# Optimization experiments

Measured on AMD Instinct MI355X. Metric: run time of the kernel, lower is better.

The kernel has to match this reference:

```python
import jax, jax.numpy as jnp
import numpy as np

N_NODES = 370
N_EEG = 64
HID = 64
L = 8
KS = 2
EMB = 16
KTOP = N_NODES // 10  # 37, as in the torch code


def _gcn_norm_dense(A):
    # A[dst, src] dense adjacency. torch_geometric GCNConv gcn_norm:
    # add self-loop weight 1.0 only for nodes lacking one, then D^-1/2 A D^-1/2.
    d0 = jnp.diagonal(A)
    A = A + jnp.diag(jnp.where(d0 > 0, 0.0, 1.0))
    deg = A.sum(axis=1)  # weighted in-degree at dst (incl. self loops)
    dinv = jnp.where(deg > 0, jax.lax.rsqrt(deg), 0.0)
    return dinv[:, None] * A * dinv[None, :]


def _adaptive_adj(emb_src, emb_tgt):
    # softmax(relu(S T^T)) row-wise, keep top-k per row (softmax vals are all >0)
    adj = jax.nn.softmax(jax.nn.relu(emb_src @ emb_tgt.T), axis=-1)
    vals, idx = jax.lax.top_k(adj, KTOP)
    sp = jnp.zeros_like(adj).at[jnp.arange(adj.shape[0])[:, None], idx].set(vals)
    return _gcn_norm_dense(sp)


def _causal_conv(h, w, b, dilation):
    # h: (BN, H, T), w: (H_out, H_in, K); left-pad by (K-1)*dilation => causal
    pad = (w.shape[-1] - 1) * dilation
    out = jax.lax.conv_general_dilated(
        h, w, window_strides=(1,), padding=[(pad, 0)],
        rhs_dilation=(dilation,), dimension_numbers=("NCH", "OIH", "NCH"))
    return out + b[None, :, None]


def _layernorm(x, g, b, eps=1e-5):
    m = x.mean(-1, keepdims=True)
    v = ((x - m) ** 2).mean(-1, keepdims=True)
    return (x - m) * jax.lax.rsqrt(v + eps) * g + b


def _gelu(x):
    return jax.nn.gelu(x, approximate=False)


def setup_inputs() -> dict:
    key = jax.random.key(0)
    ks = iter(jax.random.split(key, 64))
    B, T, E = 8, 64, 7400

    x = jax.random.normal(next(ks), (B, T, N_NODES, HID), jnp.float32)
    src = jax.random.randint(next(ks), (E,), 0, N_NODES, jnp.int32)
    off = jax.random.randint(next(ks), (E,), 1, N_NODES, jnp.int32)
    edge_index = jnp.stack([src, (src + off) % N_NODES])  # self-loop free
    edge_weight = jax.random.uniform(next(ks), (E,), jnp.float32)

    def rn(shape, scale):
        return jax.random.normal(next(ks), shape, jnp.float32) * scale

    s = 1.0 / np.sqrt(HID)
    inp = {
        "x": x, "edge_index": edge_index, "edge_weight": edge_weight,
        "in_W": rn((HID, HID), s), "in_b": rn((HID,), 0.01),
        "gcnf_W": rn((L, HID, HID), s), "gcnf_b": rn((L, HID), 0.01),
        "emb_src": rn((L, N_NODES, EMB), 1.0),  # torch.randn init
        "emb_tgt": rn((L, N_NODES, EMB), 1.0),
        "gcna_W": rn((L, HID, HID), s), "gcna_b": rn((L, HID), 0.01),
        "filt_W": rn((L, HID, HID, KS), s), "filt_b": rn((L, HID), 0.01),
        "gate_W": rn((L, HID, HID, KS), s), "gate_b": rn((L, HID), 0.01),
        "res_W": rn((L, HID, HID), s), "res_b": rn((L, HID), 0.01),
        "skip_W": rn((L, HID, HID), s), "skip_b": rn((L, HID), 0.01),
        "ln_g": jnp.ones((L, HID), jnp.float32), "ln_b": jnp.zeros((L, HID), jnp.float32),
        "end1_W": rn((HID, HID), s), "end1_b": rn((HID,), 0.01),
        "end2_W": rn((HID, HID), s), "end2_b": rn((HID,), 0.01),
        "eeg1_W": rn((N_NODES * HID, 256), 1.0 / np.sqrt(N_NODES * HID)), "eeg1_b": rn((256,), 0.01),
        "eeg2_W": rn((256, N_EEG), 1.0 / 16.0), "eeg2_b": rn((N_EEG,), 0.01),
    }
    return inp


def reference(x, edge_index, edge_weight, in_W, in_b, gcnf_W, gcnf_b,
              emb_src, emb_tgt, gcna_W, gcna_b, filt_W, filt_b, gate_W, gate_b,
              res_W, res_b, skip_W, skip_b, ln_g, ln_b,
              end1_W, end1_b, end2_W, end2_b, eeg1_W, eeg1_b, eeg2_W, eeg2_b):
    B, T, N, H = x.shape
    x = x @ in_W + in_b  # input_proj

    # Fixed (DTI prior) adjacency: same for every layer, build & normalize once.
    A = jnp.zeros((N, N), x.dtype).at[edge_index[1], edge_index[0]].add(edge_weight)
    A = _gcn_norm_dense(A)

    skip_sum = jnp.zeros_like(x)
    for i in range(L):  # fixed small layer count
        dil = 2 ** (i % 4)
        xf = x.reshape(B * T, N, H)
        h_fixed = jnp.einsum("mn,bnh->bmh", A, xf @ gcnf_W[i]) + gcnf_b[i]
        Aa = _adaptive_adj(emb_src[i], emb_tgt[i])
        h_adapt = jnp.einsum("mn,bnh->bmh", Aa, xf @ gcna_W[i]) + gcna_b[i]
        h = (h_fixed + h_adapt).reshape(B, T, N, H)
        h = h.transpose(0, 2, 3, 1).reshape(B * N, H, T)
        h = jnp.tanh(_causal_conv(h, filt_W[i], filt_b[i], dil)) * \
            jax.nn.sigmoid(_causal_conv(h, gate_W[i], gate_b[i], dil))
        # 1x1 convs over channel dim (dropout is identity in eval)
        skip = (jnp.einsum("oi,nit->not", skip_W[i], h) + skip_b[i][None, :, None])
        res = (jnp.einsum("oi,nit->not", res_W[i], h) + res_b[i][None, :, None])
        skip = skip.reshape(B, N, H, T).transpose(0, 3, 1, 2)
        res = res.reshape(B, N, H, T).transpose(0, 3, 1, 2)
        x = _layernorm(res + x, ln_g[i], ln_b[i])
        skip_sum = skip_sum + skip

    h = _gelu(skip_sum) @ end1_W + end1_b
    h = _gelu(h) @ end2_W + end2_b
    h = h.reshape(B, T, N * H)  # GraphToEEG
    h = _gelu(h @ eeg1_W + eeg1_b) @ eeg2_W + eeg2_b
    return h
```

## Files before the change

kernel.cpp:

```cpp
#include <hip/hip_runtime.h>
#include <hip/hip_bf16.h>
#include <math.h>

typedef __attribute__((ext_vector_type(8))) short bf16x8;
typedef __attribute__((ext_vector_type(4))) float f32x4;
typedef unsigned short u16;
typedef unsigned int u32;
typedef unsigned long long u64;

#define NN 370
#define HH 64
#define LL 8
#define TT 64
#define BTOT 512
#define RR (BTOT*NN)
#define KTOPK 37
#define SPLITK 37

__device__ inline u16 f2bf(float f){
  __hip_bfloat16 h = __float2bfloat16(f);
  return __builtin_bit_cast(u16, h);
}
__device__ inline float bf2f(short s){
  u32 v = ((u32)(u16)s) << 16;
  return __builtin_bit_cast(float, v);
}
__device__ inline float gelu_f(float x){ return 0.5f * x * (1.0f + erff(x * 0.70710678118654752440f)); }

__device__ inline void sts16(char* lds, int row, int kb, int stride, bf16x8 v){
  *reinterpret_cast<bf16x8*>(lds + row*stride + (kb ^ ((row&7)<<4))) = v;
}
__device__ inline bf16x8 lds16(const char* lds, int row, int kb, int stride){
  return *reinterpret_cast<const bf16x8*>(lds + row*stride + (kb ^ ((row&7)<<4)));
}
__device__ inline bf16x8 gldB(const char* Bt, int c, int kb, int stride){
  return *reinterpret_cast<const bf16x8*>(Bt + c*stride + (kb ^ ((c&7)<<4)));
}

__global__ void kzero(float* __restrict__ p, size_t n){
  for(size_t i = (size_t)blockIdx.x*256 + threadIdx.x; i < n; i += (size_t)gridDim.x*256) p[i] = 0.f;
}

__global__ void kbuildA(const int* __restrict__ ei, const float* __restrict__ ew, float* __restrict__ Araw, int E){
  int e = blockIdx.x*256 + threadIdx.x;
  if(e < E){
    int src = ei[e], dst = ei[E + e];
    atomicAdd(&Araw[dst*NN + src], ew[e]);
  }
}

__global__ __launch_bounds__(64) void knormF(float* __restrict__ Araw, float* __restrict__ dinvF){
  int i = blockIdx.x, ln = threadIdx.x;
  float d0 = Araw[i*NN + i];
  float s = 0.f;
  for(int j = ln; j < NN; j += 64) s += Araw[i*NN + j];
#pragma unroll
  for(int o=1;o<64;o<<=1) s += __shfl_xor(s, o, 64);
  if(ln == 0){
    if(d0 == 0.f){ Araw[i*NN+i] = 1.f; s += 1.f; }
    dinvF[i] = rsqrtf(s);
  }
}

__global__ __launch_bounds__(512) void kadapt(const float* __restrict__ esrc, const float* __restrict__ etgt,
                                              float* __restrict__ ArawA, float* __restrict__ dinvA){
  __shared__ float tgT[16][372];
  __shared__ float red[8];
  __shared__ u64 keys[512];
  __shared__ int diagflag;
  int i = blockIdx.x, l = blockIdx.y, tid = threadIdx.x;
  const float* Et = etgt + (size_t)l*NN*16;
  for(int idx = tid; idx < NN*16; idx += 512)
    tgT[idx & 15][idx >> 4] = Et[idx];
  float sr[16];
  const float* Es = esrc + ((size_t)l*NN + i)*16;
#pragma unroll
  for(int k=0;k<16;k++) sr[k] = Es[k];
  if(tid == 0) diagflag = 0;
  __syncthreads();
  bool act = tid < NN;
  float s = 0.f;
  if(act){
    float d = 0.f;
#pragma unroll
    for(int k=0;k<16;k++) d += sr[k]*tgT[k][tid];
    s = fmaxf(d, 0.f);
  }
  float v = act ? s : -1.f;
#pragma unroll
  for(int o=1;o<64;o<<=1) v = fmaxf(v, __shfl_xor(v,o,64));
  if((tid&63)==0) red[tid>>6] = v;
  __syncthreads();
  float mx = red[0];
#pragma unroll
  for(int q=1;q<8;q++) mx = fmaxf(mx, red[q]);
  __syncthreads();
  float e = act ? expf(s - mx) : 0.f;
  float t = e;
#pragma unroll
  for(int o=1;o<64;o<<=1) t += __shfl_xor(t,o,64);
  if((tid&63)==0) red[tid>>6] = t;
  __syncthreads();
  float sum = 0.f;
#pragma unroll
  for(int q=0;q<8;q++) sum += red[q];
  float p = e / sum;
  u32 fb = __builtin_bit_cast(u32, p);
  keys[tid] = act ? ((((u64)fb)<<32) | (u64)(0xFFFFFFFFu - (u32)tid)) : 0ULL;
  __syncthreads();
  for(int k2=2; k2<=512; k2<<=1){
    for(int j=k2>>1; j>0; j>>=1){
      int ixj = tid ^ j;
      if(ixj > tid){
        u64 a = keys[tid], b = keys[ixj];
        bool dirUp = ((tid & k2) == 0);
        if(dirUp ? (a < b) : (a > b)){ keys[tid] = b; keys[ixj] = a; }
      }
      __syncthreads();
    }
  }
  float myval = 0.f; int myidx = -1;
  if(tid < KTOPK){
    u64 kk = keys[tid];
    myidx = (int)(0xFFFFFFFFu - (u32)kk);
    myval = __builtin_bit_cast(float, (u32)(kk>>32));
    if(myidx == i) diagflag = 1;
  }
  __syncthreads();
  float dsum = (tid < KTOPK) ? myval : 0.f;
  if(tid < 64){
#pragma unroll
    for(int o=1;o<64;o<<=1) dsum += __shfl_xor(dsum,o,64);
    if(tid == 0) dinvA[l*NN + i] = rsqrtf(dsum + (diagflag ? 0.f : 1.f));
  }
  if(tid < KTOPK) ArawA[((size_t)l*NN + i)*NN + myidx] = myval;
  if(tid == 0 && !diagflag) ArawA[((size_t)l*NN + i)*NN + i] = 1.f;
}

__global__ void kacat(const float* __restrict__ Araw, const float* __restrict__ ArawA,
                      const float* __restrict__ dinvF, const float* __restrict__ dinvA,
                      u16* __restrict__ Acat){
  int idx = blockIdx.x*256 + threadIdx.x;
  if(idx >= LL*384*768) return;
  int k = idx % 768; int m = (idx / 768) % 384; int l = idx / (768*384);
  float v = 0.f;
  if(m < NN){
    if(k < 384){
      if(k < NN) v = dinvF[m]*Araw[m*NN+k]*dinvF[k];
    } else {
      int n = k - 384;
      if(n < NN) v = dinvA[l*NN+m]*ArawA[((size_t)l*NN+m)*NN+n]*dinvA[l*NN+n];
    }
  }
  Acat[idx] = f2bf(v);
}

__global__ void kbt_small(const float* __restrict__ inW, const float* __restrict__ e1W, const float* __restrict__ e2W,
                          u16* __restrict__ BtIN, u16* __restrict__ BtE1, u16* __restrict__ BtE2){
  const float* W = blockIdx.x==0 ? inW : (blockIdx.x==1 ? e1W : e2W);
  u16* Bt = blockIdx.x==0 ? BtIN : (blockIdx.x==1 ? BtE1 : BtE2);
  for(int idx = threadIdx.x; idx < 4096; idx += 256){
    int c = idx >> 6, k = idx & 63;
    *(u16*)((char*)Bt + c*128 + ((k*2) ^ ((c&7)<<4))) = f2bf(W[k*64 + c]);
  }
}

__global__ void kbt_layer(const float* __restrict__ gcnfW, const float* __restrict__ gcnaW,
                          const float* __restrict__ filtW, const float* __restrict__ gateW,
                          const float* __restrict__ skipW, const float* __restrict__ resW,
                          u16* __restrict__ BtUV, u16* __restrict__ BtCV, u16* __restrict__ BtSR){
  int l = blockIdx.x, which = blockIdx.y;
  if(which == 0){
    u16* Bt = BtUV + (size_t)l*128*64;
    for(int idx=threadIdx.x; idx<8192; idx+=256){
      int c = idx>>6, k = idx&63;
      float v = (c<64) ? gcnfW[(size_t)l*4096 + k*64 + c] : gcnaW[(size_t)l*4096 + k*64 + (c-64)];
      *(u16*)((char*)Bt + c*128 + ((k*2) ^ ((c&7)<<4))) = f2bf(v);
    }
  } else if(which == 1){
    u16* Bt = BtCV + (size_t)l*128*128;
    for(int idx=threadIdx.x; idx<16384; idx+=256){
      int c = idx>>7, k = idx&127;
      const float* W = (c<64) ? filtW : gateW;
      int o = c & 63, ii = k & 63, tap = (k<64) ? 1 : 0;
      float v = W[(size_t)l*8192 + o*128 + ii*2 + tap];
      *(u16*)((char*)Bt + c*256 + ((k*2) ^ ((c&7)<<4))) = f2bf(v);
    }
  } else {
    u16* Bt = BtSR + (size_t)l*128*64;
    for(int idx=threadIdx.x; idx<8192; idx+=256){
      int c = idx>>6, k = idx&63;
      float v = (c<64) ? skipW[(size_t)l*4096 + c*64 + k] : resW[(size_t)l*4096 + (c-64)*64 + k];
      *(u16*)((char*)Bt + c*128 + ((k*2) ^ ((c&7)<<4))) = f2bf(v);
    }
  }
}

__global__ void ktrans(const float* __restrict__ W, u16* __restrict__ Wt){
  __shared__ float tile[64][65];
  int kb = blockIdx.x*64, cb = blockIdx.y*64;
  for(int idx = threadIdx.x; idx < 4096; idx += 256){
    int kk = idx>>6, cc = idx&63;
    tile[kk][cc] = W[(size_t)(kb+kk)*256 + cb+cc];
  }
  __syncthreads();
  for(int idx = threadIdx.x; idx < 4096; idx += 256){
    int cc = idx>>6, kk = idx&63;
    Wt[(size_t)(cb+cc)*23680 + kb+kk] = f2bf(tile[kk][cc]);
  }
}

__global__ __launch_bounds__(256) void krowmm_in(const float* __restrict__ X, const u16* __restrict__ Bt,
                                                 const float* __restrict__ bias,
                                                 u16* __restrict__ xbf){
  int tid = threadIdx.x;
  int w = tid>>6, ln = tid&63, lr = ln&15, hi = ln>>4;
  int kboff = hi<<4;
  size_t r = (size_t)blockIdx.x*64 + w*16 + lr;
  f32x4 acc[4];
#pragma unroll
  for(int i=0;i<4;i++) acc[i] = f32x4{0.f,0.f,0.f,0.f};
  const char* BI = (const char*)Bt;
#pragma unroll
  for(int kt=0; kt<2; ++kt){
    const float* xr = X + r*64 + kt*32 + hi*8;
    float4 pa = ((const float4*)xr)[0], pb = ((const float4*)xr)[1];
    bf16x8 a;
    a[0]=(short)f2bf(pa.x); a[1]=(short)f2bf(pa.y); a[2]=(short)f2bf(pa.z); a[3]=(short)f2bf(pa.w);
    a[4]=(short)f2bf(pb.x); a[5]=(short)f2bf(pb.y); a[6]=(short)f2bf(pb.z); a[7]=(short)f2bf(pb.w);
#pragma unroll
    for(int nt=0; nt<4; ++nt){
      bf16x8 b = gldB(BI, nt*16 + lr, kt*64 + kboff, 128);
      acc[nt] = __builtin_amdgcn_mfma_f32_16x16x32_bf16(a, b, acc[nt], 0, 0, 0);
    }
  }
  size_t r0 = (size_t)blockIdx.x*64;
#pragma unroll
  for(int nt=0; nt<4; ++nt){
    int c = nt*16 + lr;
    float bv = bias[c];
#pragma unroll
    for(int rr=0;rr<4;++rr){
      int row = w*16 + hi*4 + rr;
      xbf[(r0+row)*64 + c] = f2bf(acc[nt][rr] + bv);
    }
  }
}

__global__ __launch_bounds__(512) void kgcn(const u16* __restrict__ xbf, const u16* __restrict__ BtUV,
                                            const u16* __restrict__ Acat,
                                            const float* __restrict__ bfb, const float* __restrict__ bab,
                                            u16* __restrict__ t2){
  __shared__ char uvt[64*768];
  int bt = blockIdx.x, tid = threadIdx.x;
  int w = tid>>6, ln = tid&63, lr = ln&15, hi = ln>>4;
  int kboff = hi<<4;
  f32x4 acc[12];
#pragma unroll
  for(int j=0;j<12;j++) acc[j] = f32x4{0.f,0.f,0.f,0.f};
  const char* xb = (const char*)(xbf + (size_t)bt*NN*64);
  for(int p=0; p<2; ++p){
    bf16x8 bw[2][4];
#pragma unroll
    for(int kt=0;kt<2;++kt)
#pragma unroll
      for(int nt=0;nt<4;++nt){
        int c = p*64 + nt*16 + lr;
        bw[kt][nt] = *reinterpret_cast<const bf16x8*>((const char*)BtUV + c*128 + ((kt*64 + kboff) ^ ((c&7)<<4)));
      }
    f32x4 uvacc[3][4];
#pragma unroll
    for(int mi=0;mi<3;++mi)
#pragma unroll
      for(int nt=0;nt<4;++nt) uvacc[mi][nt] = f32x4{0.f,0.f,0.f,0.f};
#pragma unroll
    for(int mi=0;mi<3;++mi){
      int node = (w*3+mi)*16 + lr;
#pragma unroll
      for(int kt=0;kt<2;++kt){
        bf16x8 a;
        if(node < NN) a = *reinterpret_cast<const bf16x8*>(xb + (size_t)node*128 + kt*64 + kboff);
        else { bf16x8 z = {0,0,0,0,0,0,0,0}; a = z; }
#pragma unroll
        for(int nt=0;nt<4;++nt)
          uvacc[mi][nt] = __builtin_amdgcn_mfma_f32_16x16x32_bf16(a, bw[kt][nt], uvacc[mi][nt], 0,0,0);
      }
    }
    __syncthreads();
#pragma unroll
    for(int mi=0;mi<3;++mi){
      int nd = (w*3+mi)*16 + hi*4;
#pragma unroll
      for(int nt=0;nt<4;++nt){
        int cl = nt*16 + lr;
        u64 pk = (u64)((u32)f2bf(uvacc[mi][nt][0]) | ((u32)f2bf(uvacc[mi][nt][1])<<16))
               | ((u64)((u32)f2bf(uvacc[mi][nt][2]) | ((u32)f2bf(uvacc[mi][nt][3])<<16)) << 32);
        *(u64*)(uvt + cl*768 + ((nd*2) ^ ((cl&7)<<4))) = pk;
      }
    }
    __syncthreads();
    const char* abase = (const char*)Acat + p*768 + kboff;
    __builtin_amdgcn_s_setprio(1);
#pragma unroll
    for(int kt=0; kt<12; ++kt){
      bf16x8 a0 = *reinterpret_cast<const bf16x8*>(abase + (size_t)((w*3+0)*16 + lr)*1536 + kt*64);
      bf16x8 a1 = *reinterpret_cast<const bf16x8*>(abase + (size_t)((w*3+1)*16 + lr)*1536 + kt*64);
      bf16x8 a2 = *reinterpret_cast<const bf16x8*>(abase + (size_t)((w*3+2)*16 + lr)*1536 + kt*64);
      bf16x8 b0 = lds16(uvt, 0*16 + lr, kt*64 + kboff, 768);
      bf16x8 b1 = lds16(uvt, 1*16 + lr, kt*64 + kboff, 768);
      bf16x8 b2 = lds16(uvt, 2*16 + lr, kt*64 + kboff, 768);
      bf16x8 b3 = lds16(uvt, 3*16 + lr, kt*64 + kboff, 768);
      acc[0]  = __builtin_amdgcn_mfma_f32_16x16x32_bf16(a0, b0, acc[0],  0,0,0);
      acc[1]  = __builtin_amdgcn_mfma_f32_16x16x32_bf16(a0, b1, acc[1],  0,0,0);
      acc[2]  = __builtin_amdgcn_mfma_f32_16x16x32_bf16(a0, b2, acc[2],  0,0,0);
      acc[3]  = __builtin_amdgcn_mfma_f32_16x16x32_bf16(a0, b3, acc[3],  0,0,0);
      acc[4]  = __builtin_amdgcn_mfma_f32_16x16x32_bf16(a1, b0, acc[4],  0,0,0);
      acc[5]  = __builtin_amdgcn_mfma_f32_16x16x32_bf16(a1, b1, acc[5],  0,0,0);
      acc[6]  = __builtin_amdgcn_mfma_f32_16x16x32_bf16(a1, b2, acc[6],  0,0,0);
      acc[7]  = __builtin_amdgcn_mfma_f32_16x16x32_bf16(a1, b3, acc[7],  0,0,0);
      acc[8]  = __builtin_amdgcn_mfma_f32_16x16x32_bf16(a2, b0, acc[8],  0,0,0);
      acc[9]  = __builtin_amdgcn_mfma_f32_16x16x32_bf16(a2, b1, acc[9],  0,0,0);
      acc[10] = __builtin_amdgcn_mfma_f32_16x16x32_bf16(a2, b2, acc[10], 0,0,0);
      acc[11] = __builtin_amdgcn_mfma_f32_16x16x32_bf16(a2, b3, acc[11], 0,0,0);
    }
    __builtin_amdgcn_s_setprio(0);
  }
#pragma unroll
  for(int mi=0; mi<3; ++mi){
    int mt = w*3 + mi;
    int mbase = mt*16 + hi*4;
#pragma unroll
    for(int nt=0; nt<4; ++nt){
      int col = nt*16 + lr;
      float bias = bfb[col] + bab[col];
#pragma unroll
      for(int r=0;r<4;++r){
        int m = mbase + r;
        if(m < NN) t2[((size_t)bt*NN + m)*64 + col] = f2bf(acc[mi*4+nt][r] + bias);
      }
    }
  }
}

__global__ __launch_bounds__(256) void kcsr(const u16* __restrict__ t2, const u16* __restrict__ BtC,
                                            const u16* __restrict__ BtS,
                                            const float* __restrict__ fb, const float* __restrict__ gb,
                                            const float* __restrict__ sb, const float* __restrict__ rb,
                                            const float* __restrict__ lng, const float* __restrict__ lnb,
                                            u16* __restrict__ skip,
                                            u16* __restrict__ xbf, int dil, int first, int douv){
  __shared__ char sA[24576];
  char* sact = sA;
  char* ssr  = sA + 8192;
  int blk = blockIdx.x, tid = threadIdx.x;
  int w = tid>>6, ln = tid&63, lr = ln&15, hi = ln>>4;
  int kboff = hi<<4;
  int r0 = blk*64;
  int r = r0 + w*16 + lr;
  int t = (r / NN) & (TT-1);
  const char* cur = (const char*)t2 + (size_t)r*128;
  const char* prv = cur - (size_t)dil*NN*128;
  bf16x8 a0 = *reinterpret_cast<const bf16x8*>(cur + kboff);
  bf16x8 a1 = *reinterpret_cast<const bf16x8*>(cur + 64 + kboff);
  bf16x8 a2, a3;
  if(t >= dil){
    a2 = *reinterpret_cast<const bf16x8*>(prv + kboff);
    a3 = *reinterpret_cast<const bf16x8*>(prv + 64 + kboff);
  } else {
    bf16x8 z = {0,0,0,0,0,0,0,0}; a2 = z; a3 = z;
  }
  const char* BC = (const char*)BtC;
  f32x4 acc[8];
#pragma unroll
  for(int i=0;i<8;i++) acc[i] = f32x4{0.f,0.f,0.f,0.f};
  bf16x8 afr[4] = {a0, a1, a2, a3};
#pragma unroll
  for(int kt=0; kt<4; ++kt){
    bf16x8 bfr[8];
#pragma unroll
    for(int nt=0; nt<8; ++nt)
      bfr[nt] = gldB(BC, nt*16 + lr, kt*64 + kboff, 256);
#pragma unroll
    for(int nt=0; nt<8; ++nt)
      acc[nt] = __builtin_amdgcn_mfma_f32_16x16x32_bf16(afr[kt], bfr[nt], acc[nt], 0, 0, 0);
  }
  u16 qv[4][4];
#pragma unroll
  for(int nt=0; nt<4; ++nt){
    int o = nt*16 + lr;
    float fbv = fb[o], gbv = gb[o];
#pragma unroll
    for(int rr=0;rr<4;++rr){
      float fv = acc[nt][rr] + fbv;
      float gv = acc[nt+4][rr] + gbv;
      float ef = __expf(-2.f*fv);
      float th = (1.f - ef) * __builtin_amdgcn_rcpf(1.f + ef);
      float sg = __builtin_amdgcn_rcpf(1.f + __expf(-gv));
      qv[nt][rr] = f2bf(th * sg);
    }
  }
#pragma unroll
  for(int nt=0; nt<4; ++nt){
    int col = nt*16 + lr;
#pragma unroll
    for(int rr=0;rr<4;++rr){
      int row = w*16 + hi*4 + rr;
      *(u16*)(sact + row*128 + ((col*2) ^ ((row&7)<<4))) = qv[nt][rr];
    }
  }
  __syncthreads();
  const char* BS = (const char*)BtS;
  f32x4 as[8];
#pragma unroll
  for(int i=0;i<8;i++) as[i] = f32x4{0.f,0.f,0.f,0.f};
#pragma unroll
  for(int kt=0; kt<2; ++kt){
    bf16x8 a = lds16(sact, w*16 + lr, kt*64 + kboff, 128);
    bf16x8 bfr[8];
#pragma unroll
    for(int nt=0; nt<8; ++nt)
      bfr[nt] = gldB(BS, nt*16 + lr, kt*64 + kboff, 128);
#pragma unroll
    for(int nt=0; nt<8; ++nt)
      as[nt] = __builtin_amdgcn_mfma_f32_16x16x32_bf16(a, bfr[nt], as[nt], 0, 0, 0);
  }
#pragma unroll
  for(int nt=0; nt<4; ++nt){
    int c = nt*16 + lr;
#pragma unroll
    for(int rr=0;rr<4;++rr){
      int row = w*16 + hi*4 + rr;
      *(u16*)(ssr + row*256 + (((c)*2)      ^ ((row&7)<<4))) = f2bf(as[nt][rr]);
      *(u16*)(ssr + row*256 + (((64+c)*2)   ^ ((row&7)<<4))) = f2bf(as[4+nt][rr]);
    }
  }
  __syncthreads();
  int row = tid >> 2, seg = tid & 3;
  int c0 = seg * 16;
  bf16x8 vs0 = *reinterpret_cast<const bf16x8*>(ssr + row*256 + (((c0)*2)      ^ ((row&7)<<4)));
  bf16x8 vs1 = *reinterpret_cast<const bf16x8*>(ssr + row*256 + (((c0+8)*2)    ^ ((row&7)<<4)));
  bf16x8 vr0 = *reinterpret_cast<const bf16x8*>(ssr + row*256 + (((64+c0)*2)   ^ ((row&7)<<4)));
  bf16x8 vr1 = *reinterpret_cast<const bf16x8*>(ssr + row*256 + (((64+c0+8)*2) ^ ((row&7)<<4)));
  float sk[16], re[16];
#pragma unroll
  for(int i=0;i<8;++i){ sk[i] = bf2f(vs0[i]); sk[8+i] = bf2f(vs1[i]); }
#pragma unroll
  for(int i=0;i<8;++i){ re[i] = bf2f(vr0[i]); re[8+i] = bf2f(vr1[i]); }
  size_t gr = (size_t)(r0 + row)*64 + c0;
  bf16x8 xv0 = *reinterpret_cast<const bf16x8*>(xbf + gr);
  bf16x8 xv1 = *reinterpret_cast<const bf16x8*>(xbf + gr + 8);
  float y[16]; float s1 = 0.f, s2 = 0.f;
#pragma unroll
  for(int i=0;i<16;++i){
    float xo = bf2f(i < 8 ? xv0[i] : xv1[i-8]);
    float vv = re[i] + rb[c0+i] + xo;
    y[i] = vv; s1 += vv; s2 += vv*vv;
  }
  s1 += __shfl_xor(s1, 1, 64); s1 += __shfl_xor(s1, 2, 64);
  s2 += __shfl_xor(s2, 1, 64); s2 += __shfl_xor(s2, 2, 64);
  float m = s1 * (1.f/64.f);
  float var = s2 * (1.f/64.f) - m*m;
  float rstd = rsqrtf(var + 1e-5f);
  if(douv){
    bf16x8 o0, o1;
#pragma unroll
    for(int i=0;i<16;++i){
      float xo = (y[i] - m) * rstd * lng[c0+i] + lnb[c0+i];
      if(i < 8) o0[i] = (short)f2bf(xo); else o1[i-8] = (short)f2bf(xo);
    }
    *reinterpret_cast<bf16x8*>(xbf + gr) = o0;
    *reinterpret_cast<bf16x8*>(xbf + gr + 8) = o1;
  }
  bf16x8 so0, so1;
  if(first){
#pragma unroll
    for(int i=0;i<16;++i){
      float sv = sk[i] + sb[c0+i];
      if(i < 8) so0[i] = (short)f2bf(sv); else so1[i-8] = (short)f2bf(sv);
    }
  } else {
    bf16x8 sp0 = *reinterpret_cast<const bf16x8*>(skip + gr);
    bf16x8 sp1 = *reinterpret_cast<const bf16x8*>(skip + gr + 8);
#pragma unroll
    for(int i=0;i<16;++i){
      float old = bf2f(i < 8 ? sp0[i] : sp1[i-8]);
      float sv = old + sk[i] + sb[c0+i];
      if(i < 8) so0[i] = (short)f2bf(sv); else so1[i-8] = (short)f2bf(sv);
    }
  }
  *reinterpret_cast<bf16x8*>(skip + gr) = so0;
  *reinterpret_cast<bf16x8*>(skip + gr + 8) = so1;
}

__global__ __launch_bounds__(256) void kend2(const u16* __restrict__ skip, const u16* __restrict__ Bt1,
                                             const u16* __restrict__ Bt2, const float* __restrict__ b1,
                                             const float* __restrict__ b2, u16* __restrict__ h2){
  __shared__ char sA[8192];
  int tid = threadIdx.x;
  int w = tid>>6, ln = tid&63, lr = ln&15, hi = ln>>4;
  int kboff = hi<<4;
  size_t r = (size_t)blockIdx.x*64 + w*16 + lr;
  const char* B1 = (const char*)Bt1;
  const char* B2 = (const char*)Bt2;
  f32x4 acc[4];
#pragma unroll
  for(int i=0;i<4;i++) acc[i] = f32x4{0.f,0.f,0.f,0.f};
#pragma unroll
  for(int kt=0; kt<2; ++kt){
    bf16x8 a = *reinterpret_cast<const bf16x8*>((const char*)skip + r*128 + kt*64 + kboff);
#pragma unroll
    for(int i=0;i<8;i++) a[i] = (short)f2bf(gelu_f(bf2f(a[i])));
#pragma unroll
    for(int nt=0; nt<4; ++nt){
      bf16x8 b = gldB(B1, nt*16 + lr, kt*64 + kboff, 128);
      acc[nt] = __builtin_amdgcn_mfma_f32_16x16x32_bf16(a, b, acc[nt], 0, 0, 0);
    }
  }
  u16 xq[4][4];
#pragma unroll
  for(int nt=0; nt<4; ++nt){
    int c = nt*16 + lr;
    float bv = b1[c];
#pragma unroll
    for(int rr=0;rr<4;++rr) xq[nt][rr] = f2bf(gelu_f(acc[nt][rr] + bv));
  }
#pragma unroll
  for(int nt=0; nt<4; ++nt){
    int col = nt*16 + lr;
#pragma unroll
    for(int rr=0;rr<4;++rr){
      int row = w*16 + hi*4 + rr;
      *(u16*)(sA + row*128 + ((col*2) ^ ((row&7)<<4))) = xq[nt][rr];
    }
  }
  __syncthreads();
  f32x4 a2[4];
#pragma unroll
  for(int i=0;i<4;i++) a2[i] = f32x4{0.f,0.f,0.f,0.f};
#pragma unroll
  for(int kt=0; kt<2; ++kt){
    bf16x8 a = lds16(sA, w*16 + lr, kt*64 + kboff, 128);
#pragma unroll
    for(int nt=0; nt<4; ++nt){
      bf16x8 b = gldB(B2, nt*16 + lr, kt*64 + kboff, 128);
      a2[nt] = __builtin_amdgcn_mfma_f32_16x16x32_bf16(a, b, a2[nt], 0, 0, 0);
    }
  }
  size_t rbase = (size_t)blockIdx.x*64 + w*16 + hi*4;
#pragma unroll
  for(int nt=0; nt<4; ++nt){
    int c = nt*16 + lr;
    float bv = b2[c];
#pragma unroll
    for(int rr=0;rr<4;++rr) h2[(rbase+rr)*64 + c] = f2bf(a2[nt][rr] + bv);
  }
}

__global__ __launch_bounds__(512) void keeg1(const u16* __restrict__ h2, const u16* __restrict__ WtE,
                                             float* __restrict__ part){
  __shared__ char sA[64*128];
  __shared__ char sB[256*128];
  int rowg = blockIdx.x, sp = blockIdx.y;
  int tid = threadIdx.x, w = tid>>6, ln = tid&63;
  f32x4 acc[8];
#pragma unroll
  for(int i=0;i<8;i++) acc[i] = f32x4{0.f,0.f,0.f,0.f};
  int mt = w & 3, ntb = (w>>2)*8;
  for(int ks=0; ks<20; ++ks){
    int k0 = (sp*20 + ks)*32;
    __syncthreads();
    for(int s = tid; s < 256; s += 512){
      int row = s>>2, kc = s&3;
      bf16x8 v = *reinterpret_cast<const bf16x8*>(h2 + (size_t)(rowg*64+row)*23680 + k0 + kc*8);
      sts16(sA, row, kc*16, 128, v);
    }
    for(int s = tid; s < 1024; s += 512){
      int row = s>>2, kc = s&3;
      bf16x8 v = *reinterpret_cast<const bf16x8*>(WtE + (size_t)row*23680 + k0 + kc*8);
      sts16(sB, row, kc*16, 128, v);
    }
    __syncthreads();
    bf16x8 a = lds16(sA, mt*16 + (ln&15), ((ln>>4)<<4), 128);
#pragma unroll
    for(int j=0;j<8;++j){
      bf16x8 b = lds16(sB, (ntb+j)*16 + (ln&15), ((ln>>4)<<4), 128);
      acc[j] = __builtin_amdgcn_mfma_f32_16x16x32_bf16(a, b, acc[j], 0, 0, 0);
    }
  }
  float* dst = part + ((size_t)sp*512 + rowg*64)*256;
#pragma unroll
  for(int j=0;j<8;++j){
    int c = (ntb+j)*16 + (ln&15);
#pragma unroll
    for(int r=0;r<4;++r){
      int row = mt*16 + ((ln>>4)<<2) + r;
      dst[(size_t)row*256 + c] = acc[j][r];
    }
  }
}

__global__ __launch_bounds__(256) void keeg2(const float* __restrict__ part, const float* __restrict__ b1,
                                             const float* __restrict__ W2, const float* __restrict__ b2,
                                             float* __restrict__ out){
  __shared__ float u[256];
  __shared__ float pr[4][64];
  int bt = blockIdx.x, tid = threadIdx.x;
  float sacc = 0.f;
  for(int sp2=0; sp2<SPLITK; ++sp2) sacc += part[((size_t)sp2*512 + bt)*256 + tid];
  u[tid] = gelu_f(sacc + b1[tid]);
  __syncthreads();
  int w = tid>>6, ln = tid&63;
  float acc = 0.f;
  for(int c = w*64; c < (w+1)*64; ++c) acc += u[c] * W2[c*64 + ln];
  pr[w][ln] = acc;
  __syncthreads();
  if(tid < 64)
    out[(size_t)bt*64 + tid] = pr[0][tid]+pr[1][tid]+pr[2][tid]+pr[3][tid] + b2[tid];
}

extern "C" void kernel_launch(void* const* d_in, const int* in_sizes, int n_in,
                              void* d_out, int out_size, void* d_ws, size_t ws_size,
                              hipStream_t stream){
  const float* x_in  = (const float*)d_in[0];
  const int*   ei    = (const int*)d_in[1];
  const float* ew    = (const float*)d_in[2];
  const float* in_W  = (const float*)d_in[3];
  const float* in_b  = (const float*)d_in[4];
  const float* gcnfW = (const float*)d_in[5];
  const float* gcnfb = (const float*)d_in[6];
  const float* esrc  = (const float*)d_in[7];
  const float* etgt  = (const float*)d_in[8];
  const float* gcnaW = (const float*)d_in[9];
  const float* gcnab = (const float*)d_in[10];
  const float* filtW = (const float*)d_in[11];
  const float* filtb = (const float*)d_in[12];
  const float* gateW = (const float*)d_in[13];
  const float* gateb = (const float*)d_in[14];
  const float* resW  = (const float*)d_in[15];
  const float* resb  = (const float*)d_in[16];
  const float* skipW = (const float*)d_in[17];
  const float* skipb = (const float*)d_in[18];
  const float* lng   = (const float*)d_in[19];
  const float* lnb   = (const float*)d_in[20];
  const float* e1W   = (const float*)d_in[21];
  const float* e1b   = (const float*)d_in[22];
  const float* e2W   = (const float*)d_in[23];
  const float* e2b   = (const float*)d_in[24];
  const float* eg1W  = (const float*)d_in[25];
  const float* eg1b  = (const float*)d_in[26];
  const float* eg2W  = (const float*)d_in[27];
  const float* eg2b  = (const float*)d_in[28];
  int E = in_sizes[2];

  char* p = (char*)d_ws;
  auto carve = [&](size_t bytes)->char*{ char* r = p; p += (bytes + 255) & ~(size_t)255; return r; };
  u16*   xbf   = (u16*)  carve((size_t)RR*64*2);
  u16*   skip  = (u16*)  carve((size_t)RR*64*2);
  u16*   t2    = (u16*)  carve((size_t)RR*64*2);
  u16*   h2    = (u16*)  carve((size_t)RR*64*2);
  float* Araw9 = (float*)carve((size_t)9*NN*NN*4);
  float* Araw  = Araw9;
  float* ArawA = Araw9 + (size_t)NN*NN;
  float* dinvF = (float*)carve(NN*4);
  float* dinvA = (float*)carve(LL*NN*4);
  u16*   Acat  = (u16*)  carve((size_t)LL*384*768*2);
  u16*   BtUV  = (u16*)  carve((size_t)LL*128*64*2);
  u16*   BtCV  = (u16*)  carve((size_t)LL*128*128*2);
  u16*   BtSR  = (u16*)  carve((size_t)LL*128*64*2);
  u16*   BtIN  = (u16*)  carve(64*64*2);
  u16*   BtE1  = (u16*)  carve(64*64*2);
  u16*   BtE2  = (u16*)  carve(64*64*2);
  u16*   WtE   = (u16*)  carve((size_t)256*23680*2);
  float* part  = (float*)carve((size_t)SPLITK*512*256*4);

  kzero<<<1024, 256, 0, stream>>>(Araw9, (size_t)9*NN*NN);
  kbuildA<<<(E+255)/256, 256, 0, stream>>>(ei, ew, Araw, E);
  knormF<<<NN, 64, 0, stream>>>(Araw, dinvF);
  kadapt<<<dim3(NN, LL), 512, 0, stream>>>(esrc, etgt, ArawA, dinvA);
  kacat<<<(LL*384*768 + 255)/256, 256, 0, stream>>>(Araw, ArawA, dinvF, dinvA, Acat);
  kbt_small<<<3, 256, 0, stream>>>(in_W, e1W, e2W, BtIN, BtE1, BtE2);
  kbt_layer<<<dim3(LL, 3), 256, 0, stream>>>(gcnfW, gcnaW, filtW, gateW, skipW, resW, BtUV, BtCV, BtSR);
  ktrans<<<dim3(370, 4), 256, 0, stream>>>(eg1W, WtE);

  krowmm_in<<<RR/64, 256, 0, stream>>>(x_in, BtIN, in_b, xbf);

  for(int l=0; l<LL; ++l){
    int dil = 1 << (l & 3);
    kgcn<<<BTOT, 512, 0, stream>>>(xbf, BtUV + (size_t)l*8192, Acat + (size_t)l*384*768,
                                   gcnfb + l*64, gcnab + l*64, t2);
    int douv = (l < LL-1) ? 1 : 0;
    kcsr<<<RR/64, 256, 0, stream>>>(t2, BtCV + (size_t)l*16384, BtSR + (size_t)l*8192,
                                    filtb + l*64, gateb + l*64, skipb + l*64, resb + l*64,
                                    lng + l*64, lnb + l*64, skip, xbf, dil, l==0 ? 1 : 0, douv);
  }

  kend2<<<RR/64, 256, 0, stream>>>(skip, BtE1, BtE2, e1b, e2b, h2);
  keeg1<<<dim3(8, SPLITK), 512, 0, stream>>>(h2, WtE, part);
  keeg2<<<BTOT, 256, 0, stream>>>(part, eg1b, eg2W, eg2b, (float*)d_out);
}
```

Measured before the change: 976.7 us.

## Split GCN kernel output rows across two 256-thread blocks per timestep

The graph-convolution kernel now launches two 256-thread blocks per (batch,time) slice, each computing half of the output node rows, instead of one 512-thread block. Each block still recomputes the full XW product for all nodes into shared memory (6 tiles per wave), so that work is duplicated. The aim is more blocks and better occupancy/scheduling flexibility, at the cost of redundant XW MFMA work and extra x reads.

```diff
diff --git a/kernel.cpp b/kernel.cpp
--- a/kernel.cpp
+++ b/kernel.cpp
@@ -247,12 +247,12 @@
   }
 }
 
-__global__ __launch_bounds__(512) void kgcn(const u16* __restrict__ xbf, const u16* __restrict__ BtUV,
+__global__ __launch_bounds__(256) void kgcn(const u16* __restrict__ xbf, const u16* __restrict__ BtUV,
                                             const u16* __restrict__ Acat,
                                             const float* __restrict__ bfb, const float* __restrict__ bab,
                                             u16* __restrict__ t2){
   __shared__ char uvt[64*768];
-  int bt = blockIdx.x, tid = threadIdx.x;
+  int mhalf = blockIdx.x, bt = blockIdx.y, tid = threadIdx.x;
   int w = tid>>6, ln = tid&63, lr = ln&15, hi = ln>>4;
   int kboff = hi<<4;
   f32x4 acc[12];
@@ -268,44 +268,44 @@
         int c = p*64 + nt*16 + lr;
         bw[kt][nt] = *reinterpret_cast<const bf16x8*>((const char*)BtUV + c*128 + ((kt*64 + kboff) ^ ((c&7)<<4)));
       }
-    f32x4 uvacc[3][4];
-#pragma unroll
-    for(int mi=0;mi<3;++mi)
-#pragma unroll
-      for(int nt=0;nt<4;++nt) uvacc[mi][nt] = f32x4{0.f,0.f,0.f,0.f};
-#pragma unroll
-    for(int mi=0;mi<3;++mi){
-      int node = (w*3+mi)*16 + lr;
-#pragma unroll
-      for(int kt=0;kt<2;++kt){
-        bf16x8 a;
-        if(node < NN) a = *reinterpret_cast<const bf16x8*>(xb + (size_t)node*128 + kt*64 + kboff);
-        else { bf16x8 z = {0,0,0,0,0,0,0,0}; a = z; }
-#pragma unroll
-        for(int nt=0;nt<4;++nt)
-          uvacc[mi][nt] = __builtin_amdgcn_mfma_f32_16x16x32_bf16(a, bw[kt][nt], uvacc[mi][nt], 0,0,0);
+    __syncthreads();
+#pragma unroll
+    for(int j6=0;j6<6;++j6){
+      int tile = w*6 + j6;
+      int node = tile*16 + lr;
+      bf16x8 a0, a1;
+      if(node < NN){
+        a0 = *reinterpret_cast<const bf16x8*>(xb + (size_t)node*128 + kboff);
+        a1 = *reinterpret_cast<const bf16x8*>(xb + (size_t)node*128 + 64 + kboff);
+      } else {
+        bf16x8 z = {0,0,0,0,0,0,0,0}; a0 = z; a1 = z;
       }
-    }
-    __syncthreads();
-#pragma unroll
-    for(int mi=0;mi<3;++mi){
-      int nd = (w*3+mi)*16 + hi*4;
+      f32x4 uv[4];
+#pragma unroll
+      for(int nt=0;nt<4;++nt) uv[nt] = f32x4{0.f,0.f,0.f,0.f};
+#pragma unroll
+      for(int nt=0;nt<4;++nt){
+        uv[nt] = __builtin_amdgcn_mfma_f32_16x16x32_bf16(a0, bw[0][nt], uv[nt], 0,0,0);
+        uv[nt] = __builtin_amdgcn_mfma_f32_16x16x32_bf16(a1, bw[1][nt], uv[nt], 0,0,0);
+      }
+      int nd = tile*16 + hi*4;
 #pragma unroll
       for(int nt=0;nt<4;++nt){
         int cl = nt*16 + lr;
-        u64 pk = (u64)((u32)f2bf(uvacc[mi][nt][0]) | ((u32)f2bf(uvacc[mi][nt][1])<<16))
-               | ((u64)((u32)f2bf(uvacc[mi][nt][2]) | ((u32)f2bf(uvacc[mi][nt][3])<<16)) << 32);
+        u64 pk = (u64)((u32)f2bf(uv[nt][0]) | ((u32)f2bf(uv[nt][1])<<16))
+               | ((u64)((u32)f2bf(uv[nt][2]) | ((u32)f2bf(uv[nt][3])<<16)) << 32);
         *(u64*)(uvt + cl*768 + ((nd*2) ^ ((cl&7)<<4))) = pk;
       }
     }
     __syncthreads();
+    int mb = mhalf*12 + w*3;
     const char* abase = (const char*)Acat + p*768 + kboff;
     __builtin_amdgcn_s_setprio(1);
 #pragma unroll
     for(int kt=0; kt<12; ++kt){
-      bf16x8 a0 = *reinterpret_cast<const bf16x8*>(abase + (size_t)((w*3+0)*16 + lr)*1536 + kt*64);
-      bf16x8 a1 = *reinterpret_cast<const bf16x8*>(abase + (size_t)((w*3+1)*16 + lr)*1536 + kt*64);
-      bf16x8 a2 = *reinterpret_cast<const bf16x8*>(abase + (size_t)((w*3+2)*16 + lr)*1536 + kt*64);
+      bf16x8 a0 = *reinterpret_cast<const bf16x8*>(abase + (size_t)((mb+0)*16 + lr)*1536 + kt*64);
+      bf16x8 a1 = *reinterpret_cast<const bf16x8*>(abase + (size_t)((mb+1)*16 + lr)*1536 + kt*64);
+      bf16x8 a2 = *reinterpret_cast<const bf16x8*>(abase + (size_t)((mb+2)*16 + lr)*1536 + kt*64);
       bf16x8 b0 = lds16(uvt, 0*16 + lr, kt*64 + kboff, 768);
       bf16x8 b1 = lds16(uvt, 1*16 + lr, kt*64 + kboff, 768);
       bf16x8 b2 = lds16(uvt, 2*16 + lr, kt*64 + kboff, 768);
@@ -327,7 +327,7 @@
   }
 #pragma unroll
   for(int mi=0; mi<3; ++mi){
-    int mt = w*3 + mi;
+    int mt = mhalf*12 + w*3 + mi;
     int mbase = mt*16 + hi*4;
 #pragma unroll
     for(int nt=0; nt<4; ++nt){
@@ -686,8 +686,8 @@
 
   for(int l=0; l<LL; ++l){
     int dil = 1 << (l & 3);
-    kgcn<<<BTOT, 512, 0, stream>>>(xbf, BtUV + (size_t)l*8192, Acat + (size_t)l*384*768,
-                                   gcnfb + l*64, gcnab + l*64, t2);
+    kgcn<<<dim3(2, BTOT), 256, 0, stream>>>(xbf, BtUV + (size_t)l*8192, Acat + (size_t)l*384*768,
+                                            gcnfb + l*64, gcnab + l*64, t2);
     int douv = (l < LL-1) ? 1 : 0;
     kcsr<<<RR/64, 256, 0, stream>>>(t2, BtCV + (size_t)l*16384, BtSR + (size_t)l*8192,
                                     filtb + l*64, gateb + l*64, skipb + l*64, resb + l*64,
```

Measured after the change: 1.059 ms. 8.5% more time.
